# Kernel tuning notes

Measured on AMD Instinct MI355X. Metric: run time of the kernel, lower is better.

Reference implementation:

```python
import jax, jax.numpy as jnp
import numpy as np

RPN_BBOX_STD_DEV = np.array([0.1, 0.1, 0.2, 0.2], np.float32)
PRE_NMS_LIMIT = 6000
PROPOSAL_COUNTS = 1000
NMS_THRESHOLD = 0.7
B, N = 8, 262144


def setup_inputs() -> dict:
    key = jax.random.key(0)
    k1, k2, k3, k4 = jax.random.split(key, 4)
    # rpn_class: softmax probs over {bg, fg}
    rpn_class = jax.nn.softmax(jax.random.normal(k1, (B, N, 2), dtype=jnp.float32), axis=-1)
    # rpn_bbox: small refinement deltas (pre std-dev scaling)
    rpn_bbox = jax.random.normal(k2, (B, N, 4), dtype=jnp.float32) * 0.5
    # anchors: valid normalized boxes (y1,x1,y2,x2) in [0,1]
    cy = jax.random.uniform(k3, (B, N), minval=0.05, maxval=0.95)
    cx = jax.random.uniform(jax.random.fold_in(k3, 1), (B, N), minval=0.05, maxval=0.95)
    h = jax.random.uniform(k4, (B, N), minval=0.02, maxval=0.3)
    w = jax.random.uniform(jax.random.fold_in(k4, 1), (B, N), minval=0.02, maxval=0.3)
    anchors = jnp.stack([cy - h / 2, cx - w / 2, cy + h / 2, cx + w / 2], axis=-1)
    return {"rpn_class": rpn_class, "rpn_bbox": rpn_bbox, "anchors": anchors}


def apply_box_deltas(boxes, deltas):
    # boxes, deltas: [..., 4] in (y1, x1, y2, x2) / (dy, dx, log dh, log dw)
    h = boxes[..., 2] - boxes[..., 0]
    w = boxes[..., 3] - boxes[..., 1]
    cy = boxes[..., 0] + 0.5 * h
    cx = boxes[..., 1] + 0.5 * w
    cy = cy + deltas[..., 0] * h
    cx = cx + deltas[..., 1] * w
    h = h * jnp.exp(deltas[..., 2])
    w = w * jnp.exp(deltas[..., 3])
    return jnp.stack([cy - 0.5 * h, cx - 0.5 * w, cy + 0.5 * h, cx + 0.5 * w], axis=-1)


def clip_boxes(boxes):
    # clip to normalized window [0, 0, 1, 1]
    return jnp.clip(boxes, 0.0, 1.0)


def _iou_one_vs_all(box, boxes):
    y1 = jnp.maximum(box[0], boxes[:, 0])
    x1 = jnp.maximum(box[1], boxes[:, 1])
    y2 = jnp.minimum(box[2], boxes[:, 2])
    x2 = jnp.minimum(box[3], boxes[:, 3])
    inter = jnp.maximum(y2 - y1, 0.0) * jnp.maximum(x2 - x1, 0.0)
    area1 = (box[2] - box[0]) * (box[3] - box[1])
    areas = (boxes[:, 2] - boxes[:, 0]) * (boxes[:, 3] - boxes[:, 1])
    return inter / (area1 + areas - inter + 1e-9)


def nms_pad(boxes, scores, iou_thr, max_out):
    # boxes: [K, 4], scores: [K]. Greedy NMS, zero-padded to max_out (as tf NMS + pad).
    NEG = jnp.float32(-1e9)
    k = boxes.shape[0]
    arange = jnp.arange(k)

    def step(scores_rem, _):
        idx = jnp.argmax(scores_rem)
        valid = scores_rem[idx] > NEG * 0.5
        iou = _iou_one_vs_all(boxes[idx], boxes)
        suppress = (iou > iou_thr) | (arange == idx)
        scores_new = jnp.where(suppress, NEG, scores_rem)
        return scores_new, (idx, valid)

    _, (idxs, valids) = jax.lax.scan(step, scores, None, length=max_out)
    proposals = boxes[idxs] * valids[:, None].astype(boxes.dtype)  # zero-pad invalid
    return proposals


def reference(rpn_class, rpn_bbox, anchors):
    # scores: foreground class probability
    scores = rpn_class[:, :, 1]                                    # [B, N]
    deltas = rpn_bbox * jnp.asarray(RPN_BBOX_STD_DEV).reshape(1, 1, 4)
    pre_nms_limit = min(PRE_NMS_LIMIT, anchors.shape[1])
    top_scores, ix = jax.lax.top_k(scores, pre_nms_limit)          # [B, K]
    deltas_k = jnp.take_along_axis(deltas, ix[..., None], axis=1)  # [B, K, 4]
    anchors_k = jnp.take_along_axis(anchors, ix[..., None], axis=1)
    boxes = clip_boxes(apply_box_deltas(anchors_k, deltas_k))      # [B, K, 4]
    proposals = jax.vmap(lambda b, s: nms_pad(b, s, NMS_THRESHOLD, PROPOSAL_COUNTS))(boxes, top_scores)
    return proposals                                               # [B, PROPOSAL_COUNTS, 4]
```

## Files before the change

kernel.cpp:

```cpp
#include <hip/hip_runtime.h>
#include <cstdint>
#include <math.h>

#define NBATCH 8
#define NANCH 262144
#define TOPK 6000
#define OUTK 1000
#define CAP 16384
#define ROWS 6016
#define MROWS 2048
#define MWORDS 32
#define NT2 528
#define NBIN 8192

using u32 = uint32_t;
using u64 = unsigned long long;

__device__ inline u32 binof(u64 key, u32 m) {
    u32 hb  = (u32)(key >> 52);
    u32 mid = (u32)(key >> 41) & 0x7FFu;
    u32 bi = (hb - m) * 2048u + mid;
    return bi > (NBIN - 1) ? (NBIN - 1) : bi;
}

__global__ void hist_kernel(const float* __restrict__ cls, u32* __restrict__ hist) {
    __shared__ u32 lh[4096];
    int b = blockIdx.y, t = threadIdx.x;
    for (int i = t; i < 4096; i += 256) lh[i] = 0;
    __syncthreads();
    const float4* p4 = (const float4*)(cls + (size_t)b * NANCH * 2);
    const int P = NANCH / 2;
    for (int p = blockIdx.x * 256 + t; p < P; p += gridDim.x * 256) {
        float4 v = p4[p];
        atomicAdd(&lh[__float_as_uint(v.y) >> 20], 1);
        atomicAdd(&lh[__float_as_uint(v.w) >> 20], 1);
    }
    __syncthreads();
    for (int i = t; i < 4096; i += 256) { u32 c = lh[i]; if (c) atomicAdd(&hist[b * 4096 + i], c); }
}

__global__ void compact_kernel(const float* __restrict__ cls, const u32* __restrict__ hist,
                               u32* __restrict__ meta, u64* __restrict__ cand) {
    __shared__ u64 buf[4096];
    __shared__ u32 ts[256];
    __shared__ u32 thr, lc, gbase;
    int b = blockIdx.y, t = threadIdx.x;
    if (t == 0) lc = 0;
    const u32* h = hist + b * 4096;
    u32 s = 0;
    for (int k = 0; k < 16; k++) s += h[t * 16 + k];
    ts[t] = s; __syncthreads();
    u32 suf = 0;
    for (int t2 = t + 1; t2 < 256; t2++) suf += ts[t2];
    if (suf < TOPK && suf + s >= TOPK) {
        u32 a = suf;
        for (int k = 15; k >= 0; k--) {
            u32 c = h[t * 16 + k];
            if (a + c >= TOPK) { thr = (u32)(t * 16 + k) << 20; break; }
            a += c;
        }
    }
    __syncthreads();
    u32 T = thr;
    if (t == 0) meta[56 + b] = T >> 20;
    const float4* p4 = (const float4*)(cls + (size_t)b * NANCH * 2);
    const int P = NANCH / 2;
    for (int p = blockIdx.x * 256 + t; p < P; p += gridDim.x * 256) {
        float4 v = p4[p];
        u32 k0 = __float_as_uint(v.y), k1 = __float_as_uint(v.w);
        u32 n0 = 2u * (u32)p, n1 = n0 + 1u;
        if (k0 >= T) { u32 q = atomicAdd(&lc, 1u); buf[q] = ((u64)k0 << 32) | (u32)(~n0); }
        if (k1 >= T) { u32 q = atomicAdd(&lc, 1u); buf[q] = ((u64)k1 << 32) | (u32)(~n1); }
    }
    __syncthreads();
    if (t == 0) gbase = atomicAdd(&meta[48 + b], lc);
    __syncthreads();
    u32 base = gbase, n = lc;
    for (u32 j = t; j < n; j += 256) {
        u32 d = base + j;
        if (d < CAP) cand[(size_t)b * CAP + d] = buf[j];
    }
}

__global__ __launch_bounds__(1024) void group_kernel(
                            const u64* __restrict__ cand, const u32* __restrict__ meta,
                            u64* __restrict__ grouped) {
    __shared__ u32 lh[NBIN];
    __shared__ u32 part[1024];
    __shared__ u32 wsum[16];
    int b = blockIdx.x, t = threadIdx.x;
    int wv = t >> 6, l = t & 63;
    u32 cnt = meta[48 + b]; if (cnt > CAP) cnt = CAP;
    u32 m = meta[56 + b];
    const u64* cb = cand + (size_t)b * CAP;
    u64* gb = grouped + (size_t)b * CAP;
    #pragma unroll
    for (int k = 0; k < NBIN / 1024; k++) lh[t + k * 1024] = 0;
    __syncthreads();
    for (u32 i = t; i < cnt; i += 1024) atomicAdd(&lh[binof(cb[i], m)], 1u);
    __syncthreads();
    u32 s = 0;
    #pragma unroll
    for (int k = 0; k < 8; k++) s += lh[t * 8 + k];
    part[t] = s;
    __syncthreads();
    u32 wsuf = 0;
    for (int k = l + 1; k < 64; k++) wsuf += part[(wv << 6) + k];
    if (l == 0) wsum[wv] = wsuf + part[wv << 6];
    __syncthreads();
    u32 cur = wsuf;
    for (int k = wv + 1; k < 16; k++) cur += wsum[k];
    #pragma unroll
    for (int k = 7; k >= 0; k--) {
        u32 c = lh[t * 8 + k];
        lh[t * 8 + k] = cur;
        cur += c;
    }
    __syncthreads();
    for (u32 i = t; i < cnt; i += 1024) {
        u64 key = cb[i];
        u32 p = atomicAdd(&lh[binof(key, m)], 1u);
        if (p < CAP) gb[p] = key;
    }
}

__global__ __launch_bounds__(256) void rank_kernel(
                            const u64* __restrict__ grouped, const u32* __restrict__ meta,
                            const float* __restrict__ anchors, const float* __restrict__ bbox,
                            float4* __restrict__ boxes, float* __restrict__ areas) {
    int b = blockIdx.y, t = threadIdx.x;
    int p = blockIdx.x * 256 + t;
    u32 cnt = meta[48 + b]; if (cnt > CAP) cnt = CAP;
    if (blockIdx.x == 0 && t < ROWS - TOPK) {
        boxes[(size_t)b * ROWS + TOPK + t] = make_float4(0.f, 0.f, 0.f, 0.f);
        areas[(size_t)b * ROWS + TOPK + t] = 0.f;
    }
    if (p >= (int)cnt) return;
    u32 m = meta[56 + b];
    const u64* gb = grouped + (size_t)b * CAP;
    u64 key = gb[p];
    u32 bi = binof(key, m);
    int s = p;
    while (s > 0 && binof(gb[s - 1], m) == bi) s--;
    u32 r = 0;
    int q = s;
    while (q < (int)cnt) {
        u64 kq = gb[q];
        if (binof(kq, m) != bi) break;
        r += (kq > key) ? 1u : 0u;
        q++;
    }
    u32 rank = (u32)s + r;
    if (rank < TOPK) {
        u32 idx = ~(u32)(key & 0xFFFFFFFFull);
        size_t off = ((size_t)b * NANCH + idx) * 4;
        const float4 a = *(const float4*)(anchors + off);
        const float4 d = *(const float4*)(bbox + off);
        float h = a.z - a.x, w = a.w - a.y;
        float cy = a.x + 0.5f * h, cx = a.y + 0.5f * w;
        float dy = d.x * 0.1f, dx = d.y * 0.1f, dh = d.z * 0.2f, dw = d.w * 0.2f;
        cy = cy + dy * h; cx = cx + dx * w;
        h = h * (float)exp((double)dh);
        w = w * (float)exp((double)dw);
        float y1 = cy - 0.5f * h, x1 = cx - 0.5f * w;
        float y2 = cy + 0.5f * h, x2 = cx + 0.5f * w;
        y1 = fminf(fmaxf(y1, 0.f), 1.f); x1 = fminf(fmaxf(x1, 0.f), 1.f);
        y2 = fminf(fmaxf(y2, 0.f), 1.f); x2 = fminf(fmaxf(x2, 0.f), 1.f);
        boxes[(size_t)b * ROWS + rank] = make_float4(y1, x1, y2, x2);
        areas[(size_t)b * ROWS + rank] = (y2 - y1) * (x2 - x1);
    }
}

__device__ inline u64 wave_or64(u64 x) {
    u32 lo = (u32)x, hi = (u32)(x >> 32);
    lo |= __builtin_amdgcn_ds_swizzle(lo, 0x041F); hi |= __builtin_amdgcn_ds_swizzle(hi, 0x041F);
    lo |= __builtin_amdgcn_ds_swizzle(lo, 0x081F); hi |= __builtin_amdgcn_ds_swizzle(hi, 0x081F);
    lo |= __builtin_amdgcn_ds_swizzle(lo, 0x101F); hi |= __builtin_amdgcn_ds_swizzle(hi, 0x101F);
    lo |= __builtin_amdgcn_ds_swizzle(lo, 0x201F); hi |= __builtin_amdgcn_ds_swizzle(hi, 0x201F);
    lo |= __builtin_amdgcn_ds_swizzle(lo, 0x401F); hi |= __builtin_amdgcn_ds_swizzle(hi, 0x401F);
    u32 l0 = (u32)__builtin_amdgcn_readlane((int)lo, 0)  | (u32)__builtin_amdgcn_readlane((int)lo, 32);
    u32 h0 = (u32)__builtin_amdgcn_readlane((int)hi, 0)  | (u32)__builtin_amdgcn_readlane((int)hi, 32);
    return ((u64)h0 << 32) | l0;
}

__global__ __launch_bounds__(256) void nms_mask_kernel(const float4* __restrict__ boxes,
                                                       const float* __restrict__ areas,
                                                       u64* __restrict__ Mt) {
    const float  EPS  = 3.8146972656e-06f;
    const double MIDD = (double)0.7f + 2.9802322387695312e-08;
    __shared__ float4 scol[4][64];
    __shared__ float  sare[4][64];
    int b = blockIdx.y;
    int wv = threadIdx.x >> 6, l = threadIdx.x & 63;
    int tid = blockIdx.x * 4 + wv;
    if (tid >= NT2) return;
    int cb = (int)((sqrt(8.0 * (double)tid + 1.0) - 1.0) * 0.5);
    while ((cb + 1) * (cb + 2) / 2 <= tid) cb++;
    while (cb * (cb + 1) / 2 > tid) cb--;
    int rt = tid - cb * (cb + 1) / 2;
    const float4* bx = boxes + (size_t)b * ROWS;
    const float*  ar = areas + (size_t)b * ROWS;
    scol[wv][l] = bx[cb * 64 + l];
    sare[wv][l] = ar[cb * 64 + l];
    int row = rt * 64 + l;
    float4 r4 = bx[row];
    float  rar = ar[row];
    u32 wlo = 0, whi = 0; u64 unc = 0;
    #pragma unroll
    for (int c = 63; c >= 0; c--) {
        float4 c4 = scol[wv][c];
        float  caf = sare[wv][c];
        float y1 = fmaxf(r4.x, c4.x), x1 = fmaxf(r4.y, c4.y);
        float y2 = fminf(r4.z, c4.z), x2 = fminf(r4.w, c4.w);
        float inter = fmaxf(y2 - y1, 0.f) * fmaxf(x2 - x1, 0.f);
        float uni = ((rar + caf) - inter) + 1e-9f;
        float d = fmaf(uni, -0.7f, inter);
        float tt = uni * EPS;
        u32 sup = (d > tt) ? 1u : 0u;
        unc |= __ballot(fabsf(d) <= tt);
        if (c >= 32) whi = (whi << 1) | sup;
        else         wlo = (wlo << 1) | sup;
    }
    if (unc) {
        wlo = 0; whi = 0;
        for (int c = 63; c >= 0; c--) {
            float4 c4 = scol[wv][c]; float caf = sare[wv][c];
            float y1 = fmaxf(r4.x, c4.x), x1 = fmaxf(r4.y, c4.y);
            float y2 = fminf(r4.z, c4.z), x2 = fminf(r4.w, c4.w);
            float inter = fmaxf(y2 - y1, 0.f) * fmaxf(x2 - x1, 0.f);
            float uni = ((rar + caf) - inter) + 1e-9f;
            double td = fma((double)uni, -MIDD, (double)inter);
            u32 sup = (td >= 0.0) ? 1u : 0u;
            if (c >= 32) whi = (whi << 1) | sup;
            else         wlo = (wlo << 1) | sup;
        }
    }
    u64 w = ((u64)whi << 32) | wlo;
    if (cb == rt) {
        w &= (l < 63) ? (~0ull << (l + 1)) : 0ull;
        u64 tw = 0;
        for (int c2 = 0; c2 < 64; c2++) {
            u64 bc = __ballot((u32)((w >> c2) & 1ull) != 0u);
            if (l == c2) tw = bc;
        }
        w = tw | (1ull << l);
    }
    Mt[((size_t)b * MWORDS + cb) * MROWS + row] = w;
}

__global__ __launch_bounds__(64) void nms_seq_kernel(const float4* __restrict__ boxes,
                                                     const float* __restrict__ areas,
                                                     const u64* __restrict__ Mt,
                                                     float* __restrict__ out) {
    const double MIDD = (double)0.7f + 2.9802322387695312e-08;
    __shared__ u32 keptIdx[1024];
    __shared__ float4 sbox[1024];
    __shared__ float  skar[1024];
    int b = blockIdx.x, l = threadIdx.x;
    const u64* Mb = Mt + (size_t)b * MWORDS * MROWS;
    const float4* bx = boxes + (size_t)b * ROWS;
    const float*  ar = areas + (size_t)b * ROWS;
    float4* ob = (float4*)(out + (size_t)b * OUTK * 4);
    const u64 below = (1ull << l) - 1ull;
    int kept = 0;
    u64 rw = 0;
    u64 dw0 = Mb[l];
    float4 vb0 = bx[l];  float va0 = ar[l];
    u64 X0 = Mb[(size_t)MROWS + l];
    u64 dw1 = Mb[(size_t)MROWS + 64 + l];
    float4 vb1 = bx[64 + l]; float va1 = ar[64 + l];
    u64 X1 = Mb[(size_t)2 * MROWS + 64 + l];
    u64 gp = 0;
    for (int c = 0; c < MWORDS; c++) {
        int base = c * 64;
        u64 alive = ~rw;
        u64 K = alive;
        while (true) {
            u64 Kn = alive & ~__ballot((dw0 & K & below) != 0ull);
            if (Kn == K) break;
            K = Kn;
        }
        int avail = OUTK - kept;
        int nk  = (int)__popcll(K);
        int pos = (int)__popcll(K & below);
        u32 keptme = (u32)((K >> l) & 1ull);
        if (nk > avail) keptme &= (u32)(pos < avail);
        if (keptme) {
            int opos = kept + pos;
            ob[opos] = vb0;
            keptIdx[opos] = (u32)(base + l);
            sbox[opos] = vb0;
            skar[opos] = va0;
        }
        kept += (nk < avail) ? nk : avail;
        if (kept >= OUTK || c + 1 >= MWORDS) break;
        rw = wave_or64((keptme ? X0 : 0ull) | gp);
        __syncthreads();
        u64 dw2 = 0, X2 = 0; float4 vb2 = make_float4(0.f, 0.f, 0.f, 0.f); float va2 = 0.f;
        u64 gpn = 0;
        if (c + 2 < MWORDS) {
            int nb2 = base + 128;
            dw2 = Mb[(size_t)(c + 2) * MROWS + nb2 + l];
            vb2 = bx[nb2 + l]; va2 = ar[nb2 + l];
            if (c + 3 < MWORDS) X2 = Mb[(size_t)(c + 3) * MROWS + nb2 + l];
            int K2g = kept;
            if (K2g > 0) {
                #pragma unroll
                for (int u = 0; u < 16; u++) {
                    int k = l + (u << 6);
                    u32 idx = keptIdx[(k < K2g) ? k : K2g - 1];
                    gpn |= Mb[(size_t)(c + 2) * MROWS + idx];
                }
            }
        }
        dw0 = dw1; X0 = X1; vb0 = vb1; va0 = va1;
        dw1 = dw2; X1 = X2; vb1 = vb2; va1 = va2;
        gp = gpn;
    }
    if (kept < OUTK) {
        __syncthreads();
        for (int i = MROWS; i < TOPK && kept < OUTK; i++) {
            float4 c4 = bx[i]; float ca = ar[i];
            int sup = 0;
            for (int j = l; j < kept; j += 64) {
                float4 kb = sbox[j]; float ka = skar[j];
                float y1 = fmaxf(kb.x, c4.x), x1 = fmaxf(kb.y, c4.y);
                float y2 = fminf(kb.z, c4.z), x2 = fminf(kb.w, c4.w);
                float inter = fmaxf(y2 - y1, 0.f) * fmaxf(x2 - x1, 0.f);
                float uni = ((ka + ca) - inter) + 1e-9f;
                double td = fma((double)uni, -MIDD, (double)inter);
                sup |= (td >= 0.0) ? 1 : 0;
            }
            if (!__any(sup)) {
                if (l == 0) { ob[kept] = c4; sbox[kept] = c4; skar[kept] = ca; }
                kept++;
            }
        }
    }
    for (int p = kept + l; p < OUTK; p += 64)
        ob[p] = make_float4(0.f, 0.f, 0.f, 0.f);
}

extern "C" void kernel_launch(void* const* d_in, const int* in_sizes, int n_in,
                              void* d_out, int out_size, void* d_ws, size_t ws_size,
                              hipStream_t stream) {
    const float* cls     = (const float*)d_in[0];
    const float* bbox    = (const float*)d_in[1];
    const float* anchors = (const float*)d_in[2];

    char* ws = (char*)d_ws;
    u32* hist1 = (u32*)(ws);
    u32* meta  = (u32*)(ws + 131072);
    float4* boxes = (float4*)(ws + 131328);
    float* areas  = (float*)(ws + 901376);
    u64* Mt = (u64*)(ws + 1093888);
    u64* cand    = (u64*)(ws + 1093888);
    u64* grouped = (u64*)(ws + 1093888 + 1048576);
    size_t need = 1093888 + (size_t)NBATCH * MWORDS * MROWS * 8;
    if (ws_size < need) return;

    hipMemsetAsync(ws, 0, 131328, stream);

    hist_kernel<<<dim3(64, NBATCH), 256, 0, stream>>>(cls, hist1);
    compact_kernel<<<dim3(64, NBATCH), 256, 0, stream>>>(cls, hist1, meta, cand);
    group_kernel<<<NBATCH, 1024, 0, stream>>>(cand, meta, grouped);
    rank_kernel<<<dim3(CAP / 256, NBATCH), 256, 0, stream>>>(grouped, meta, anchors, bbox, boxes, areas);
    nms_mask_kernel<<<dim3((NT2 + 3) / 4, NBATCH), 256, 0, stream>>>(boxes, areas, Mt);
    nms_seq_kernel<<<NBATCH, 64, 0, stream>>>(boxes, areas, Mt, (float*)d_out);
}
```

Before: 175.6 us.

## Fuse compact+group and mask+seq kernels using last-block-done atomic counters

Merges the compaction and grouping kernels into one launch, and likewise the NMS mask and sequential-selection kernels. In each, the last block to finish (found by an atomic counter in meta plus threadfences) runs the follow-on stage. This removes two kernel launches and their inter-kernel gaps. The cost is that the grouping stage now runs with 256 threads instead of 1024, and the serial NMS runs inside a 256-thread block where only one wave is active.

Measured after the change: 221.1 us. 1.26x slower.

```diff
diff --git a/kernel.cpp b/kernel.cpp
--- a/kernel.cpp
+++ b/kernel.cpp
@@ -16,11 +16,24 @@
 using u32 = uint32_t;
 using u64 = unsigned long long;
 
+
 __device__ inline u32 binof(u64 key, u32 m) {
     u32 hb  = (u32)(key >> 52);
     u32 mid = (u32)(key >> 41) & 0x7FFu;
     u32 bi = (hb - m) * 2048u + mid;
     return bi > (NBIN - 1) ? (NBIN - 1) : bi;
+}
+
+__device__ inline u64 wave_or64(u64 x) {
+    u32 lo = (u32)x, hi = (u32)(x >> 32);
+    lo |= __builtin_amdgcn_ds_swizzle(lo, 0x041F); hi |= __builtin_amdgcn_ds_swizzle(hi, 0x041F);
+    lo |= __builtin_amdgcn_ds_swizzle(lo, 0x081F); hi |= __builtin_amdgcn_ds_swizzle(hi, 0x081F);
+    lo |= __builtin_amdgcn_ds_swizzle(lo, 0x101F); hi |= __builtin_amdgcn_ds_swizzle(hi, 0x101F);
+    lo |= __builtin_amdgcn_ds_swizzle(lo, 0x201F); hi |= __builtin_amdgcn_ds_swizzle(hi, 0x201F);
+    lo |= __builtin_amdgcn_ds_swizzle(lo, 0x401F); hi |= __builtin_amdgcn_ds_swizzle(hi, 0x401F);
+    u32 l0 = (u32)__builtin_amdgcn_readlane((int)lo, 0)  | (u32)__builtin_amdgcn_readlane((int)lo, 32);
+    u32 h0 = (u32)__builtin_amdgcn_readlane((int)hi, 0)  | (u32)__builtin_amdgcn_readlane((int)hi, 32);
+    return ((u64)h0 << 32) | l0;
 }
 
 __global__ void hist_kernel(const float* __restrict__ cls, u32* __restrict__ hist) {
@@ -39,13 +52,15 @@
     for (int i = t; i < 4096; i += 256) { u32 c = lh[i]; if (c) atomicAdd(&hist[b * 4096 + i], c); }
 }
 
-__global__ void compact_kernel(const float* __restrict__ cls, const u32* __restrict__ hist,
-                               u32* __restrict__ meta, u64* __restrict__ cand) {
-    __shared__ u64 buf[4096];
-    __shared__ u32 ts[256];
-    __shared__ u32 thr, lc, gbase;
+__global__ __launch_bounds__(256) void compact_group_kernel(
+        const float* __restrict__ cls, const u32* __restrict__ hist,
+        u32* __restrict__ meta, u64* __restrict__ cand, u64* __restrict__ grouped) {
+    __shared__ alignas(16) char smem[34816];
+    u64* buf = (u64*)smem;
+    u32* ts  = (u32*)(smem + 32768);
+    u32* sc  = (u32*)(smem + 33792);
     int b = blockIdx.y, t = threadIdx.x;
-    if (t == 0) lc = 0;
+    if (t == 0) sc[1] = 0;
     const u32* h = hist + b * 4096;
     u32 s = 0;
     for (int k = 0; k < 16; k++) s += h[t * 16 + k];
@@ -56,68 +71,70 @@
         u32 a = suf;
         for (int k = 15; k >= 0; k--) {
             u32 c = h[t * 16 + k];
-            if (a + c >= TOPK) { thr = (u32)(t * 16 + k) << 20; break; }
+            if (a + c >= TOPK) { sc[0] = (u32)(t * 16 + k) << 20; break; }
             a += c;
         }
     }
     __syncthreads();
-    u32 T = thr;
-    if (t == 0) meta[56 + b] = T >> 20;
+    u32 T = sc[0];
+    if (t == 0 && blockIdx.x == 0) meta[56 + b] = T >> 20;
     const float4* p4 = (const float4*)(cls + (size_t)b * NANCH * 2);
     const int P = NANCH / 2;
-    for (int p = blockIdx.x * 256 + t; p < P; p += gridDim.x * 256) {
+    for (int p = blockIdx.x * 256 + t; p < P; p += 64 * 256) {
         float4 v = p4[p];
         u32 k0 = __float_as_uint(v.y), k1 = __float_as_uint(v.w);
         u32 n0 = 2u * (u32)p, n1 = n0 + 1u;
-        if (k0 >= T) { u32 q = atomicAdd(&lc, 1u); buf[q] = ((u64)k0 << 32) | (u32)(~n0); }
-        if (k1 >= T) { u32 q = atomicAdd(&lc, 1u); buf[q] = ((u64)k1 << 32) | (u32)(~n1); }
-    }
-    __syncthreads();
-    if (t == 0) gbase = atomicAdd(&meta[48 + b], lc);
-    __syncthreads();
-    u32 base = gbase, n = lc;
+        if (k0 >= T) { u32 q = atomicAdd(&sc[1], 1u); buf[q] = ((u64)k0 << 32) | (u32)(~n0); }
+        if (k1 >= T) { u32 q = atomicAdd(&sc[1], 1u); buf[q] = ((u64)k1 << 32) | (u32)(~n1); }
+    }
+    __syncthreads();
+    if (t == 0) sc[2] = atomicAdd(&meta[48 + b], sc[1]);
+    __syncthreads();
+    u32 base = sc[2], n = sc[1];
     for (u32 j = t; j < n; j += 256) {
         u32 d = base + j;
         if (d < CAP) cand[(size_t)b * CAP + d] = buf[j];
     }
-}
-
-__global__ __launch_bounds__(1024) void group_kernel(
-                            const u64* __restrict__ cand, const u32* __restrict__ meta,
-                            u64* __restrict__ grouped) {
-    __shared__ u32 lh[NBIN];
-    __shared__ u32 part[1024];
-    __shared__ u32 wsum[16];
-    int b = blockIdx.x, t = threadIdx.x;
+    __syncthreads();
+    if (t == 0) {
+        __threadfence();
+        sc[3] = (atomicAdd(&meta[b], 1u) == 63u) ? 1u : 0u;
+    }
+    __syncthreads();
+    if (!sc[3]) return;
+    __threadfence();
+    u32* lh   = (u32*)smem;
+    u32* part = (u32*)(smem + 32768);
+    u32* wsum = (u32*)(smem + 33824);
     int wv = t >> 6, l = t & 63;
     u32 cnt = meta[48 + b]; if (cnt > CAP) cnt = CAP;
     u32 m = meta[56 + b];
     const u64* cb = cand + (size_t)b * CAP;
     u64* gb = grouped + (size_t)b * CAP;
     #pragma unroll
-    for (int k = 0; k < NBIN / 1024; k++) lh[t + k * 1024] = 0;
-    __syncthreads();
-    for (u32 i = t; i < cnt; i += 1024) atomicAdd(&lh[binof(cb[i], m)], 1u);
-    __syncthreads();
-    u32 s = 0;
+    for (int k = 0; k < 32; k++) lh[t + (k << 8)] = 0;
+    __syncthreads();
+    for (u32 i = t; i < cnt; i += 256) atomicAdd(&lh[binof(cb[i], m)], 1u);
+    __syncthreads();
+    u32 s2 = 0;
     #pragma unroll
-    for (int k = 0; k < 8; k++) s += lh[t * 8 + k];
-    part[t] = s;
+    for (int k = 0; k < 32; k++) s2 += lh[t * 32 + k];
+    part[t] = s2;
     __syncthreads();
     u32 wsuf = 0;
     for (int k = l + 1; k < 64; k++) wsuf += part[(wv << 6) + k];
     if (l == 0) wsum[wv] = wsuf + part[wv << 6];
     __syncthreads();
     u32 cur = wsuf;
-    for (int k = wv + 1; k < 16; k++) cur += wsum[k];
+    for (int k = wv + 1; k < 4; k++) cur += wsum[k];
     #pragma unroll
-    for (int k = 7; k >= 0; k--) {
-        u32 c = lh[t * 8 + k];
-        lh[t * 8 + k] = cur;
+    for (int k = 31; k >= 0; k--) {
+        u32 c = lh[t * 32 + k];
+        lh[t * 32 + k] = cur;
         cur += c;
     }
     __syncthreads();
-    for (u32 i = t; i < cnt; i += 1024) {
+    for (u32 i = t; i < cnt; i += 256) {
         u64 key = cb[i];
         u32 p = atomicAdd(&lh[binof(key, m)], 1u);
         if (p < CAP) gb[p] = key;
@@ -171,174 +188,165 @@
     }
 }
 
-__device__ inline u64 wave_or64(u64 x) {
-    u32 lo = (u32)x, hi = (u32)(x >> 32);
-    lo |= __builtin_amdgcn_ds_swizzle(lo, 0x041F); hi |= __builtin_amdgcn_ds_swizzle(hi, 0x041F);
-    lo |= __builtin_amdgcn_ds_swizzle(lo, 0x081F); hi |= __builtin_amdgcn_ds_swizzle(hi, 0x081F);
-    lo |= __builtin_amdgcn_ds_swizzle(lo, 0x101F); hi |= __builtin_amdgcn_ds_swizzle(hi, 0x101F);
-    lo |= __builtin_amdgcn_ds_swizzle(lo, 0x201F); hi |= __builtin_amdgcn_ds_swizzle(hi, 0x201F);
-    lo |= __builtin_amdgcn_ds_swizzle(lo, 0x401F); hi |= __builtin_amdgcn_ds_swizzle(hi, 0x401F);
-    u32 l0 = (u32)__builtin_amdgcn_readlane((int)lo, 0)  | (u32)__builtin_amdgcn_readlane((int)lo, 32);
-    u32 h0 = (u32)__builtin_amdgcn_readlane((int)hi, 0)  | (u32)__builtin_amdgcn_readlane((int)hi, 32);
-    return ((u64)h0 << 32) | l0;
-}
-
-__global__ __launch_bounds__(256) void nms_mask_kernel(const float4* __restrict__ boxes,
-                                                       const float* __restrict__ areas,
-                                                       u64* __restrict__ Mt) {
+__global__ __launch_bounds__(256) void nms_mask_seq_kernel(
+        const float4* __restrict__ boxes, const float* __restrict__ areas,
+        u32* __restrict__ meta, u64* __restrict__ Mt, float* __restrict__ out) {
     const float  EPS  = 3.8146972656e-06f;
     const double MIDD = (double)0.7f + 2.9802322387695312e-08;
-    __shared__ float4 scol[4][64];
-    __shared__ float  sare[4][64];
-    int b = blockIdx.y;
-    int wv = threadIdx.x >> 6, l = threadIdx.x & 63;
+    __shared__ alignas(16) char smem[24832];
+    __shared__ u32 lastf;
+    float4* scol = (float4*)smem;
+    float*  sare = (float*)(smem + 4096);
+    int b = blockIdx.y, t = threadIdx.x;
+    int wv = t >> 6, l = t & 63;
     int tid = blockIdx.x * 4 + wv;
-    if (tid >= NT2) return;
-    int cb = (int)((sqrt(8.0 * (double)tid + 1.0) - 1.0) * 0.5);
-    while ((cb + 1) * (cb + 2) / 2 <= tid) cb++;
-    while (cb * (cb + 1) / 2 > tid) cb--;
-    int rt = tid - cb * (cb + 1) / 2;
-    const float4* bx = boxes + (size_t)b * ROWS;
-    const float*  ar = areas + (size_t)b * ROWS;
-    scol[wv][l] = bx[cb * 64 + l];
-    sare[wv][l] = ar[cb * 64 + l];
-    int row = rt * 64 + l;
-    float4 r4 = bx[row];
-    float  rar = ar[row];
-    u32 wlo = 0, whi = 0; u64 unc = 0;
-    #pragma unroll
-    for (int c = 63; c >= 0; c--) {
-        float4 c4 = scol[wv][c];
-        float  caf = sare[wv][c];
-        float y1 = fmaxf(r4.x, c4.x), x1 = fmaxf(r4.y, c4.y);
-        float y2 = fminf(r4.z, c4.z), x2 = fminf(r4.w, c4.w);
-        float inter = fmaxf(y2 - y1, 0.f) * fmaxf(x2 - x1, 0.f);
-        float uni = ((rar + caf) - inter) + 1e-9f;
-        float d = fmaf(uni, -0.7f, inter);
-        float tt = uni * EPS;
-        u32 sup = (d > tt) ? 1u : 0u;
-        unc |= __ballot(fabsf(d) <= tt);
-        if (c >= 32) whi = (whi << 1) | sup;
-        else         wlo = (wlo << 1) | sup;
-    }
-    if (unc) {
-        wlo = 0; whi = 0;
+    {
+        int cbt = (int)((sqrt(8.0 * (double)tid + 1.0) - 1.0) * 0.5);
+        while ((cbt + 1) * (cbt + 2) / 2 <= tid) cbt++;
+        while (cbt * (cbt + 1) / 2 > tid) cbt--;
+        int rt = tid - cbt * (cbt + 1) / 2;
+        const float4* bx = boxes + (size_t)b * ROWS;
+        const float*  ar = areas + (size_t)b * ROWS;
+        scol[(wv << 6) + l] = bx[cbt * 64 + l];
+        sare[(wv << 6) + l] = ar[cbt * 64 + l];
+        int row = rt * 64 + l;
+        float4 r4 = bx[row];
+        float  rar = ar[row];
+        u32 wlo = 0, whi = 0; u64 unc = 0;
+        #pragma unroll
         for (int c = 63; c >= 0; c--) {
-            float4 c4 = scol[wv][c]; float caf = sare[wv][c];
+            float4 c4 = scol[(wv << 6) + c];
+            float  caf = sare[(wv << 6) + c];
             float y1 = fmaxf(r4.x, c4.x), x1 = fmaxf(r4.y, c4.y);
             float y2 = fminf(r4.z, c4.z), x2 = fminf(r4.w, c4.w);
             float inter = fmaxf(y2 - y1, 0.f) * fmaxf(x2 - x1, 0.f);
             float uni = ((rar + caf) - inter) + 1e-9f;
-            double td = fma((double)uni, -MIDD, (double)inter);
-            u32 sup = (td >= 0.0) ? 1u : 0u;
+            float d = fmaf(uni, -0.7f, inter);
+            float tt = uni * EPS;
+            u32 sup = (d > tt) ? 1u : 0u;
+            unc |= __ballot(fabsf(d) <= tt);
             if (c >= 32) whi = (whi << 1) | sup;
             else         wlo = (wlo << 1) | sup;
         }
-    }
-    u64 w = ((u64)whi << 32) | wlo;
-    if (cb == rt) {
-        w &= (l < 63) ? (~0ull << (l + 1)) : 0ull;
-        u64 tw = 0;
-        for (int c2 = 0; c2 < 64; c2++) {
-            u64 bc = __ballot((u32)((w >> c2) & 1ull) != 0u);
-            if (l == c2) tw = bc;
-        }
-        w = tw | (1ull << l);
-    }
-    Mt[((size_t)b * MWORDS + cb) * MROWS + row] = w;
-}
-
-__global__ __launch_bounds__(64) void nms_seq_kernel(const float4* __restrict__ boxes,
-                                                     const float* __restrict__ areas,
-                                                     const u64* __restrict__ Mt,
-                                                     float* __restrict__ out) {
-    const double MIDD = (double)0.7f + 2.9802322387695312e-08;
-    __shared__ u32 keptIdx[1024];
-    __shared__ float4 sbox[1024];
-    __shared__ float  skar[1024];
-    int b = blockIdx.x, l = threadIdx.x;
-    const u64* Mb = Mt + (size_t)b * MWORDS * MROWS;
-    const float4* bx = boxes + (size_t)b * ROWS;
-    const float*  ar = areas + (size_t)b * ROWS;
-    float4* ob = (float4*)(out + (size_t)b * OUTK * 4);
-    const u64 below = (1ull << l) - 1ull;
-    int kept = 0;
-    u64 rw = 0;
-    u64 dw0 = Mb[l];
-    float4 vb0 = bx[l];  float va0 = ar[l];
-    u64 X0 = Mb[(size_t)MROWS + l];
-    u64 dw1 = Mb[(size_t)MROWS + 64 + l];
-    float4 vb1 = bx[64 + l]; float va1 = ar[64 + l];
-    u64 X1 = Mb[(size_t)2 * MROWS + 64 + l];
-    u64 gp = 0;
-    for (int c = 0; c < MWORDS; c++) {
-        int base = c * 64;
-        u64 alive = ~rw;
-        u64 K = alive;
-        while (true) {
-            u64 Kn = alive & ~__ballot((dw0 & K & below) != 0ull);
-            if (Kn == K) break;
-            K = Kn;
-        }
-        int avail = OUTK - kept;
-        int nk  = (int)__popcll(K);
-        int pos = (int)__popcll(K & below);
-        u32 keptme = (u32)((K >> l) & 1ull);
-        if (nk > avail) keptme &= (u32)(pos < avail);
-        if (keptme) {
-            int opos = kept + pos;
-            ob[opos] = vb0;
-            keptIdx[opos] = (u32)(base + l);
-            sbox[opos] = vb0;
-            skar[opos] = va0;
-        }
-        kept += (nk < avail) ? nk : avail;
-        if (kept >= OUTK || c + 1 >= MWORDS) break;
-        rw = wave_or64((keptme ? X0 : 0ull) | gp);
-        __syncthreads();
-        u64 dw2 = 0, X2 = 0; float4 vb2 = make_float4(0.f, 0.f, 0.f, 0.f); float va2 = 0.f;
-        u64 gpn = 0;
-        if (c + 2 < MWORDS) {
-            int nb2 = base + 128;
-            dw2 = Mb[(size_t)(c + 2) * MROWS + nb2 + l];
-            vb2 = bx[nb2 + l]; va2 = ar[nb2 + l];
-            if (c + 3 < MWORDS) X2 = Mb[(size_t)(c + 3) * MROWS + nb2 + l];
-            int K2g = kept;
-            if (K2g > 0) {
-                #pragma unroll
-                for (int u = 0; u < 16; u++) {
-                    int k = l + (u << 6);
-                    u32 idx = keptIdx[(k < K2g) ? k : K2g - 1];
-                    gpn |= Mb[(size_t)(c + 2) * MROWS + idx];
+        if (unc) {
+            wlo = 0; whi = 0;
+            for (int c = 63; c >= 0; c--) {
+                float4 c4 = scol[(wv << 6) + c]; float caf = sare[(wv << 6) + c];
+                float y1 = fmaxf(r4.x, c4.x), x1 = fmaxf(r4.y, c4.y);
+                float y2 = fminf(r4.z, c4.z), x2 = fminf(r4.w, c4.w);
+                float inter = fmaxf(y2 - y1, 0.f) * fmaxf(x2 - x1, 0.f);
+                float uni = ((rar + caf) - inter) + 1e-9f;
+                double td = fma((double)uni, -MIDD, (double)inter);
+                u32 sup = (td >= 0.0) ? 1u : 0u;
+                if (c >= 32) whi = (whi << 1) | sup;
+                else         wlo = (wlo << 1) | sup;
+            }
+        }
+        u64 w = ((u64)whi << 32) | wlo;
+        if (cbt == rt) {
+            w &= (l < 63) ? (~0ull << (l + 1)) : 0ull;
+            u64 tw = 0;
+            for (int c2 = 0; c2 < 64; c2++) {
+                u64 bc = __ballot((u32)((w >> c2) & 1ull) != 0u);
+                if (l == c2) tw = bc;
+            }
+            w = tw | (1ull << l);
+        }
+        Mt[((size_t)b * MWORDS + cbt) * MROWS + row] = w;
+    }
+    __syncthreads();
+    if (t == 0) {
+        __threadfence();
+        lastf = (atomicAdd(&meta[8 + b], 1u) == (u32)(NT2 / 4 - 1)) ? 1u : 0u;
+    }
+    __syncthreads();
+    if (!lastf || t >= 64) return;
+    __threadfence();
+    {
+        u32*    keptIdx = (u32*)smem;
+        float4* sbox    = (float4*)(smem + 4096);
+        float*  skar    = (float*)(smem + 20480);
+        const u64* Mb = Mt + (size_t)b * MWORDS * MROWS;
+        const float4* bx = boxes + (size_t)b * ROWS;
+        const float*  ar = areas + (size_t)b * ROWS;
+        float4* ob = (float4*)(out + (size_t)b * OUTK * 4);
+        const u64 below = (1ull << l) - 1ull;
+        int kept = 0;
+        u64 rw = 0;
+        u64 dw0 = Mb[l];
+        float4 vb0 = bx[l];  float va0 = ar[l];
+        u64 X0 = Mb[(size_t)MROWS + l];
+        u64 dw1 = Mb[(size_t)MROWS + 64 + l];
+        float4 vb1 = bx[64 + l]; float va1 = ar[64 + l];
+        u64 X1 = Mb[(size_t)2 * MROWS + 64 + l];
+        u64 gp = 0;
+        for (int c = 0; c < MWORDS; c++) {
+            int base = c * 64;
+            u64 alive = ~rw;
+            u64 K = alive;
+            while (true) {
+                u64 Kn = alive & ~__ballot((dw0 & K & below) != 0ull);
+                if (Kn == K) break;
+                K = Kn;
+            }
+            int avail = OUTK - kept;
+            int nk  = (int)__popcll(K);
+            int pos = (int)__popcll(K & below);
+            u32 keptme = (u32)((K >> l) & 1ull);
+            if (nk > avail) keptme &= (u32)(pos < avail);
+            if (keptme) {
+                int opos = kept + pos;
+                ob[opos] = vb0;
+                keptIdx[opos] = (u32)(base + l);
+                sbox[opos] = vb0;
+                skar[opos] = va0;
+            }
+            kept += (nk < avail) ? nk : avail;
+            if (kept >= OUTK || c + 1 >= MWORDS) break;
+            rw = wave_or64((keptme ? X0 : 0ull) | gp);
+            u64 dw2 = 0, X2 = 0; float4 vb2 = make_float4(0.f, 0.f, 0.f, 0.f); float va2 = 0.f;
+            u64 gpn = 0;
+            if (c + 2 < MWORDS) {
+                int nb2 = base + 128;
+                dw2 = Mb[(size_t)(c + 2) * MROWS + nb2 + l];
+                vb2 = bx[nb2 + l]; va2 = ar[nb2 + l];
+                if (c + 3 < MWORDS) X2 = Mb[(size_t)(c + 3) * MROWS + nb2 + l];
+                int K2g = kept;
+                if (K2g > 0) {
+                    #pragma unroll
+                    for (int u = 0; u < 16; u++) {
+                        int k = l + (u << 6);
+                        u32 idx = keptIdx[(k < K2g) ? k : K2g - 1];
+                        gpn |= Mb[(size_t)(c + 2) * MROWS + idx];
+                    }
                 }
             }
-        }
-        dw0 = dw1; X0 = X1; vb0 = vb1; va0 = va1;
-        dw1 = dw2; X1 = X2; vb1 = vb2; va1 = va2;
-        gp = gpn;
-    }
-    if (kept < OUTK) {
-        __syncthreads();
-        for (int i = MROWS; i < TOPK && kept < OUTK; i++) {
-            float4 c4 = bx[i]; float ca = ar[i];
-            int sup = 0;
-            for (int j = l; j < kept; j += 64) {
-                float4 kb = sbox[j]; float ka = skar[j];
-                float y1 = fmaxf(kb.x, c4.x), x1 = fmaxf(kb.y, c4.y);
-                float y2 = fminf(kb.z, c4.z), x2 = fminf(kb.w, c4.w);
-                float inter = fmaxf(y2 - y1, 0.f) * fmaxf(x2 - x1, 0.f);
-                float uni = ((ka + ca) - inter) + 1e-9f;
-                double td = fma((double)uni, -MIDD, (double)inter);
-                sup |= (td >= 0.0) ? 1 : 0;
-            }
-            if (!__any(sup)) {
-                if (l == 0) { ob[kept] = c4; sbox[kept] = c4; skar[kept] = ca; }
-                kept++;
-            }
-        }
-    }
-    for (int p = kept + l; p < OUTK; p += 64)
-        ob[p] = make_float4(0.f, 0.f, 0.f, 0.f);
+            dw0 = dw1; X0 = X1; vb0 = vb1; va0 = va1;
+            dw1 = dw2; X1 = X2; vb1 = vb2; va1 = va2;
+            gp = gpn;
+        }
+        if (kept < OUTK) {
+            for (int i = MROWS; i < TOPK && kept < OUTK; i++) {
+                float4 c4 = bx[i]; float ca = ar[i];
+                int sup = 0;
+                for (int j = l; j < kept; j += 64) {
+                    float4 kb = sbox[j]; float ka = skar[j];
+                    float y1 = fmaxf(kb.x, c4.x), x1 = fmaxf(kb.y, c4.y);
+                    float y2 = fminf(kb.z, c4.z), x2 = fminf(kb.w, c4.w);
+                    float inter = fmaxf(y2 - y1, 0.f) * fmaxf(x2 - x1, 0.f);
+                    float uni = ((ka + ca) - inter) + 1e-9f;
+                    double td = fma((double)uni, -MIDD, (double)inter);
+                    sup |= (td >= 0.0) ? 1 : 0;
+                }
+                if (!__any(sup)) {
+                    if (l == 0) { ob[kept] = c4; sbox[kept] = c4; skar[kept] = ca; }
+                    kept++;
+                }
+            }
+        }
+        for (int p = kept + l; p < OUTK; p += 64)
+            ob[p] = make_float4(0.f, 0.f, 0.f, 0.f);
+    }
 }
 
 extern "C" void kernel_launch(void* const* d_in, const int* in_sizes, int n_in,
@@ -362,9 +370,7 @@
     hipMemsetAsync(ws, 0, 131328, stream);
 
     hist_kernel<<<dim3(64, NBATCH), 256, 0, stream>>>(cls, hist1);
-    compact_kernel<<<dim3(64, NBATCH), 256, 0, stream>>>(cls, hist1, meta, cand);
-    group_kernel<<<NBATCH, 1024, 0, stream>>>(cand, meta, grouped);
+    compact_group_kernel<<<dim3(64, NBATCH), 256, 0, stream>>>(cls, hist1, meta, cand, grouped);
     rank_kernel<<<dim3(CAP / 256, NBATCH), 256, 0, stream>>>(grouped, meta, anchors, bbox, boxes, areas);
-    nms_mask_kernel<<<dim3((NT2 + 3) / 4, NBATCH), 256, 0, stream>>>(boxes, areas, Mt);
-    nms_seq_kernel<<<NBATCH, 64, 0, stream>>>(boxes, areas, Mt, (float*)d_out);
-}
+    nms_mask_seq_kernel<<<dim3(NT2 / 4, NBATCH), 256, 0, stream>>>(boxes, areas, meta, Mt, (float*)d_out);
+}
```
